# Optimization experiments

Hardware: AMD Instinct MI355X
Metric: run time of the kernel (lower is better)

Reference implementation:

```python
import jax, jax.numpy as jnp
import numpy as np

N = 20000          # nodes
DEG = 8            # deterministic in-degree per node
E = N * DEG        # edges
IN_DIM = 16
HID = 128
EDGE_DIM = 8
OUT_DIM = 4
LN_EPS = 1e-5
# degree histogram has all mass at DEG -> avg log-degree = log(DEG + 1)
AVG_DEG_LOG = float(np.log(DEG + 1.0))


def _init(key, fan_in, fan_out):
    s = float(np.sqrt(2.0 / (fan_in + fan_out)))  # glorot-ish
    return jax.random.normal(key, (fan_in, fan_out), jnp.float32) * s


def setup_inputs() -> dict:
    key = jax.random.key(0)
    ks = jax.random.split(key, 24)
    x = jax.random.normal(ks[0], (N, IN_DIM), jnp.float32)
    src = jax.random.randint(ks[1], (E,), 0, N, jnp.int32)
    dst = (jnp.arange(E, dtype=jnp.int32) % N)  # every node has exactly DEG in-edges
    edge_index = jnp.stack([src, dst], axis=0)
    edge_attr = jax.random.normal(ks[2], (E, EDGE_DIM), jnp.float32)
    d = {"x": x, "edge_attr": edge_attr, "edge_index": edge_index}
    i = 3
    for l, fi in enumerate([IN_DIM, HID]):  # 2 PNAConv layers (num_layers=3)
        d[f"ew{l}"] = _init(ks[i], EDGE_DIM, fi); i += 1   # edge_encoder
        d[f"eb{l}"] = jnp.zeros((fi,), jnp.float32)
        d[f"pw{l}"] = _init(ks[i], 3 * fi, fi); i += 1     # pre_nn: cat(x_i,x_j,e)
        d[f"pb{l}"] = jnp.zeros((fi,), jnp.float32)
        d[f"qw{l}"] = _init(ks[i], 13 * fi, HID); i += 1   # post_nn: (4 aggr * 3 scalers + 1)*F_in
        d[f"qb{l}"] = jnp.zeros((HID,), jnp.float32)
        d[f"lw{l}"] = _init(ks[i], HID, HID); i += 1       # PNAConv.lin
        d[f"lb{l}"] = jnp.zeros((HID,), jnp.float32)
        d[f"g{l}"] = jnp.ones((HID,), jnp.float32)         # LayerNorm gamma
        d[f"b{l}"] = jnp.zeros((HID,), jnp.float32)        # LayerNorm beta
    d["hw"] = _init(ks[i], HID, OUT_DIM)
    d["hb"] = jnp.zeros((OUT_DIM,), jnp.float32)
    return d


def _pna_conv(x, src, dst, edge_attr, ew, eb, pw, pb, qw, qb, lw, lb):
    # messages: cat(x_i, x_j, edge_encoder(edge_attr)) -> pre MLP
    e = edge_attr @ ew + eb                                   # [E, F_in]
    h = jnp.concatenate([x[dst], x[src], e], axis=-1)         # [E, 3*F_in]
    h = h @ pw + pb                                           # [E, F_in]
    # multi-aggregator reduce by destination node
    deg = jax.ops.segment_sum(jnp.ones((E,), h.dtype), dst, num_segments=N)
    degc = jnp.maximum(deg, 1.0)[:, None]
    mean = jax.ops.segment_sum(h, dst, num_segments=N) / degc
    mean2 = jax.ops.segment_sum(h * h, dst, num_segments=N) / degc
    mx = jax.ops.segment_max(h, dst, num_segments=N)
    mn = jax.ops.segment_min(h, dst, num_segments=N)
    std = jnp.sqrt(jax.nn.relu(mean2 - mean * mean) + 1e-5)
    agg = jnp.concatenate([mean, mx, mn, std], axis=-1)       # [N, 4*F_in]
    # degree scalers: identity, amplification, attenuation (scaler-major layout)
    logd = jnp.log(deg + 1.0)[:, None]
    scaled = jnp.concatenate(
        [agg, agg * (logd / AVG_DEG_LOG), agg * (AVG_DEG_LOG / logd)], axis=-1
    )                                                         # [N, 12*F_in]
    out = jnp.concatenate([x, scaled], axis=-1) @ qw + qb     # post_nn, [N, F_out]
    return out @ lw + lb                                      # PNAConv.lin


def _ln(x, g, b):
    m = jnp.mean(x, axis=-1, keepdims=True)
    v = jnp.mean((x - m) ** 2, axis=-1, keepdims=True)
    return (x - m) / jnp.sqrt(v + LN_EPS) * g + b


def reference(x, edge_attr, ew0, eb0, pw0, pb0, qw0, qb0, lw0, lb0, g0, b0,
              ew1, eb1, pw1, pb1, qw1, qb1, lw1, lb1, g1, b1, hw, hb, edge_index):
    src, dst = edge_index[0], edge_index[1]
    h = _pna_conv(x, src, dst, edge_attr, ew0, eb0, pw0, pb0, qw0, qb0, lw0, lb0)
    h = jax.nn.relu(_ln(h, g0, b0))  # dropout is identity at inference
    h = _pna_conv(h, src, dst, edge_attr, ew1, eb1, pw1, pb1, qw1, qb1, lw1, lb1)
    h = jax.nn.relu(_ln(h, g1, b1))
    return h @ hw + hb               # head, [N, OUT_DIM]
```

## Files before the change

### kernel.cpp

```cpp
#include <hip/hip_runtime.h>
#include <math.h>

#define N_NODES 20000
#define N_EDGES 160000

typedef unsigned short ushort_t;
typedef __attribute__((ext_vector_type(8))) short short8v;
typedef __attribute__((ext_vector_type(4))) float f32x4;

#define WS_We0  0
#define WS_b0m  128
#define WS_W0   256
#define WS_b0   10496
#define WS_We1  10624
#define WS_b1m  11648
#define WS_b1   11776
#define WS_WP1  11904
#define WS_WPTU 52864
#define WS_t0   69248
#define WS_u0   389248
#define WS_h0b  709248
#define WS_t1   1989248
#define WS_u1   4549248
#define WS_A0   7109248
#define WS_A1   7109248

__device__ inline ushort_t f2bf(float f) {
    union { float f; unsigned u; } v; v.f = f;
    unsigned r = v.u + 0x7FFFu + ((v.u >> 16) & 1u);
    return (ushort_t)(r >> 16);
}
__device__ inline float bf2f(short s) {
    union { unsigned u; float f; } v; v.u = ((unsigned)(ushort_t)s) << 16; return v.f;
}

__device__ __attribute__((noinline)) void prep_item(
    int tid, const float* __restrict__ x,
    const float* __restrict__ ew0, const float* __restrict__ eb0,
    const float* __restrict__ pw0, const float* __restrict__ pb0,
    const float* __restrict__ qw0, const float* __restrict__ qb0,
    const float* __restrict__ lw0, const float* __restrict__ lb0,
    const float* __restrict__ ew1, const float* __restrict__ eb1,
    const float* __restrict__ pw1, const float* __restrict__ pb1,
    const float* __restrict__ qw1, const float* __restrict__ qb1,
    const float* __restrict__ lw1, const float* __restrict__ lb1,
    float* __restrict__ ws)
{
    if (tid < 81920) {
        int r = tid >> 7, o = tid & 127;
        float acc = 0.f;
        for (int h = 0; h < 128; ++h) {
            float qr;
            if (r < 128) qr = qw1[r*128 + h];
            else {
                int s = r - 128;
                qr = qw1[(128+s)*128+h] + qw1[(640+s)*128+h] + qw1[(1152+s)*128+h];
            }
            acc += qr * lw1[h*128 + o];
        }
        int ct = o >> 4, ks = r >> 5;
        int l = (o & 15) | (((r >> 3) & 3) << 4);
        ((ushort_t*)(ws + WS_WP1))[(size_t)(((ct*20 + ks)*64) + l)*8 + (r & 7)] = f2bf(acc);
    } else if (tid < 82048) {
        int o = tid - 81920;
        float acc = lb1[o];
        for (int h = 0; h < 128; ++h) acc += qb1[h] * lw1[h*128 + o];
        ws[WS_b1 + o] = acc;
    } else if (tid < 92288) {
        int idx = tid - 82048; int r = idx >> 7, o = idx & 127;
        float acc = 0.f;
        for (int h = 0; h < 128; ++h) {
            float qr;
            if (r < 16) qr = qw0[r*128 + h];
            else {
                int s = r - 16;
                qr = qw0[(16+s)*128+h] + qw0[(80+s)*128+h] + qw0[(144+s)*128+h];
            }
            acc += qr * lw0[h*128 + o];
        }
        ws[WS_W0 + idx] = acc;
    } else if (tid < 92416) {
        int o = tid - 92288;
        float acc = lb0[o];
        for (int h = 0; h < 128; ++h) acc += qb0[h] * lw0[h*128 + o];
        ws[WS_b0 + o] = acc;
    } else if (tid < 93440) {
        int idx = tid - 92416; int c = idx >> 7, f = idx & 127;
        float acc = 0.f;
        for (int k = 0; k < 128; ++k) acc += ew1[c*128 + k] * pw1[(256+k)*128 + f];
        ws[WS_We1 + idx] = acc;
    } else if (tid < 93568) {
        int f = tid - 93440;
        float acc = pb1[f];
        for (int k = 0; k < 128; ++k) acc += eb1[k] * pw1[(256+k)*128 + f];
        ws[WS_b1m + f] = acc;
    } else if (tid < 93696) {
        int idx = tid - 93568; int c = idx >> 4, f = idx & 15;
        float acc = 0.f;
        for (int k = 0; k < 16; ++k) acc += ew0[c*16 + k] * pw0[(32+k)*16 + f];
        ws[WS_We0 + idx] = acc;
    } else if (tid < 93712) {
        int f = tid - 93696;
        float acc = pb0[f];
        for (int k = 0; k < 16; ++k) acc += eb0[k] * pw0[(32+k)*16 + f];
        ws[WS_b0m + f] = acc;
    } else if (tid < 126480) {
        int idx = tid - 93712;
        int r = idx >> 7, o = idx & 127;
        int part = r >> 7, rk = r & 127;
        int ct = part*8 + (o >> 4);
        int l = (o & 15) | (((rk >> 3) & 3) << 4);
        ((ushort_t*)(ws + WS_WPTU))[(size_t)(((ct*4 + (rk >> 5))*64) + l)*8 + (rk & 7)]
            = f2bf(pw1[r*128 + o]);
    } else if (tid < 446480) {
        int idx = tid - 126480; int i = idx >> 4, f = idx & 15;
        float acc = 0.f;
        for (int k = 0; k < 16; ++k) acc += x[i*16 + k] * pw0[k*16 + f];
        ws[WS_t0 + idx] = acc;
    } else if (tid < 766480) {
        int idx = tid - 446480; int i = idx >> 4, f = idx & 15;
        float acc = 0.f;
        for (int k = 0; k < 16; ++k) acc += x[i*16 + k] * pw0[(16+k)*16 + f];
        ws[WS_u0 + idx] = acc;
    }
}

__device__ __attribute__((noinline)) void agg0_tile(
    int tile, int t, const float* __restrict__ x, const float* __restrict__ ea,
    const int* __restrict__ src, float* __restrict__ ws)
{
    static __shared__ float ea_s0[16*8*8];
    static __shared__ int   src_s0[16*8];
    static __shared__ float We0_s0[128];
    static __shared__ float b0m_s0[16];
    const int i0 = tile * 16;
    __syncthreads();

    for (int idx = t; idx < 1024; idx += 256) {
        int k = idx >> 7; int rem = idx & 127; int n = rem >> 3, c = rem & 7;
        ea_s0[(n*8 + k)*8 + c] = ea[(i0 + n + k*N_NODES)*8 + c];
    }
    if (t < 128) {
        int k = t >> 4, n = t & 15;
        src_s0[n*8 + k] = src[i0 + n + k*N_NODES];
        We0_s0[t] = ws[WS_We0 + t];
    }
    if (t < 16) b0m_s0[t] = ws[WS_b0m + t];
    __syncthreads();

    const int n = t >> 4, f = t & 15;
    const int i = i0 + n;
    float base = ws[WS_t0 + i*16 + f] + b0m_s0[f];
    float s = 0.f, q = 0.f, mx = -1e30f, mn = 1e30f;
    for (int k = 0; k < 8; ++k) {
        int sj = src_s0[n*8 + k];
        float m = base + ws[WS_u0 + sj*16 + f];
        #pragma unroll
        for (int c = 0; c < 8; ++c) m += ea_s0[(n*8+k)*8 + c] * We0_s0[c*16 + f];
        s += m; q += m*m; mx = fmaxf(mx, m); mn = fminf(mn, m);
    }
    float mean = s * 0.125f, mean2 = q * 0.125f;
    float sd = sqrtf(fmaxf(mean2 - mean*mean, 0.f) + 1e-5f);
    float* A0 = ws + WS_A0 + (size_t)i * 80;
    A0[f]      = x[i*16 + f];
    A0[16 + f] = mean;
    A0[32 + f] = mx;
    A0[48 + f] = mn;
    A0[64 + f] = sd;
}

__device__ __attribute__((noinline)) void gemm0_tile(
    int tile, int t, const float* __restrict__ g0, const float* __restrict__ bln0,
    float* __restrict__ ws)
{
    static __shared__ float As[32][81];
    const int r0 = tile * 32;
    __syncthreads();
    const float* A = ws + WS_A0 + (size_t)r0 * 80;
    for (int idx = t; idx < 32*80; idx += 256) {
        int r = idx / 80, k = idx - r*80;
        As[r][k] = A[idx];
    }
    __syncthreads();
    const int tc = t & 31, tr = t >> 5;
    const int c0 = tc * 4;
    float acc[4][4] = {};
    const float* W = ws + WS_W0;
    #pragma unroll 4
    for (int k = 0; k < 80; ++k) {
        float4 b = *(const float4*)(W + k*128 + c0);
        #pragma unroll
        for (int rr = 0; rr < 4; ++rr) {
            float a = As[tr*4 + rr][k];
            acc[rr][0] += a*b.x; acc[rr][1] += a*b.y;
            acc[rr][2] += a*b.z; acc[rr][3] += a*b.w;
        }
    }
    float4 bias = *(const float4*)(ws + WS_b0 + c0);
    float4 g  = *(const float4*)(g0 + c0);
    float4 bb = *(const float4*)(bln0 + c0);
    ushort_t* h0b = (ushort_t*)(ws + WS_h0b);
    #pragma unroll
    for (int rr = 0; rr < 4; ++rr) {
        float v0 = acc[rr][0] + bias.x, v1 = acc[rr][1] + bias.y;
        float v2 = acc[rr][2] + bias.z, v3 = acc[rr][3] + bias.w;
        float sum = v0+v1+v2+v3;
        float sq  = v0*v0+v1*v1+v2*v2+v3*v3;
        #pragma unroll
        for (int off = 1; off < 32; off <<= 1) {
            sum += __shfl_xor(sum, off, 64);
            sq  += __shfl_xor(sq,  off, 64);
        }
        float mean = sum * (1.f/128.f);
        float var  = sq  * (1.f/128.f) - mean*mean;
        float rstd = rsqrtf(var + 1e-5f);
        ushort4 ob;
        ob.x = f2bf(fmaxf((v0-mean)*rstd*g.x + bb.x, 0.f));
        ob.y = f2bf(fmaxf((v1-mean)*rstd*g.y + bb.y, 0.f));
        ob.z = f2bf(fmaxf((v2-mean)*rstd*g.z + bb.z, 0.f));
        ob.w = f2bf(fmaxf((v3-mean)*rstd*g.w + bb.w, 0.f));
        *(ushort4*)(h0b + (size_t)(r0 + tr*4 + rr)*128 + c0) = ob;
    }
}

__device__ __attribute__((noinline)) void tu1_half(
    int tile, int part, int lane, float* __restrict__ ws)
{
    const int rowbase = tile * 16;
    const ushort_t* h0b = (const ushort_t*)(ws + WS_h0b);
    const ushort_t* WP  = (const ushort_t*)(ws + WS_WPTU);
    const int lr = lane & 15, lk = lane >> 4;
    const size_t arow = rowbase + lr;
    f32x4 acc[8];
    #pragma unroll
    for (int c = 0; c < 8; ++c) acc[c] = (f32x4){0.f,0.f,0.f,0.f};

    #pragma unroll
    for (int ks = 0; ks < 4; ++ks) {
        short8v a = *(const short8v*)(h0b + arow*128 + ks*32 + lk*8);
        #pragma unroll
        for (int c = 0; c < 8; ++c) {
            short8v b = *(const short8v*)(WP + ((size_t)((part*8 + c)*4 + ks)*64 + lane)*8);
            acc[c] = __builtin_amdgcn_mfma_f32_16x16x32_bf16(a, b, acc[c], 0, 0, 0);
        }
    }
    if (part == 0) {
        float* t1 = ws + WS_t1;
        #pragma unroll
        for (int c = 0; c < 8; ++c) {
            int cb = c*16 + lr;
            #pragma unroll
            for (int r = 0; r < 4; ++r) {
                int row = rowbase + lk*4 + r;
                t1[(size_t)row*128 + cb] = acc[c][r];
            }
        }
    } else {
        ushort_t* u1b = (ushort_t*)(ws + WS_u1);
        #pragma unroll
        for (int c = 0; c < 8; ++c) {
            int cb = c*16 + lr;
            #pragma unroll
            for (int r = 0; r < 4; ++r) {
                int row = rowbase + lk*4 + r;
                u1b[(size_t)row*128 + cb] = f2bf(acc[c][r]);
            }
        }
    }
}

__device__ __attribute__((noinline)) void agg1_tile(
    int tile, int t, const float* __restrict__ ea, const int* __restrict__ src,
    float* __restrict__ ws)
{
    static __shared__ float ea_s1[16*8*8];
    static __shared__ int   src_s1[128];
    static __shared__ float We1_s1[1024];
    static __shared__ float b1m_s1[128];
    const int i0 = tile * 16;
    __syncthreads();

    for (int idx = t; idx < 1024; idx += 256) {
        int k = idx >> 7; int rem = idx & 127; int n = rem >> 3, c = rem & 7;
        ea_s1[(n*8 + k)*8 + c] = ea[(i0 + n + k*N_NODES)*8 + c];
    }
    if (t < 128) {
        int k = t >> 4, n = t & 15;
        src_s1[n*8 + k] = src[i0 + n + k*N_NODES];
    }
    for (int idx = t; idx < 1024; idx += 256) We1_s1[idx] = ws[WS_We1 + idx];
    if (t < 128) b1m_s1[t] = ws[WS_b1m + t];
    __syncthreads();

    const int n = t >> 4, f0 = (t & 15) * 8;
    const int i = i0 + n;
    const ushort_t* u1b = (const ushort_t*)(ws + WS_u1);
    float base[8], sm[8], sq[8], mx[8], mn[8];
    #pragma unroll
    for (int e = 0; e < 8; ++e) {
        base[e] = ws[WS_t1 + (size_t)i*128 + f0 + e] + b1m_s1[f0 + e];
        sm[e] = 0.f; sq[e] = 0.f; mx[e] = -1e30f; mn[e] = 1e30f;
    }
    for (int k = 0; k < 8; ++k) {
        int sj = src_s1[n*8 + k];
        short8v uv = *(const short8v*)(u1b + (size_t)sj*128 + f0);
        float m[8];
        #pragma unroll
        for (int e = 0; e < 8; ++e) m[e] = base[e] + bf2f(uv[e]);
        #pragma unroll
        for (int c = 0; c < 8; ++c) {
            float a = ea_s1[(n*8 + k)*8 + c];
            #pragma unroll
            for (int e = 0; e < 8; ++e) m[e] += a * We1_s1[c*128 + f0 + e];
        }
        #pragma unroll
        for (int e = 0; e < 8; ++e) {
            sm[e] += m[e]; sq[e] += m[e]*m[e];
            mx[e] = fmaxf(mx[e], m[e]); mn[e] = fminf(mn[e], m[e]);
        }
    }
    ushort_t* A1 = (ushort_t*)(ws + WS_A1);
    short8v vm, vx, vn, vs;
    #pragma unroll
    for (int e = 0; e < 8; ++e) {
        float mean = sm[e]*0.125f, m2 = sq[e]*0.125f;
        float sd = sqrtf(fmaxf(m2 - mean*mean, 0.f) + 1e-5f);
        vm[e] = (short)f2bf(mean);
        vx[e] = (short)f2bf(mx[e]);
        vn[e] = (short)f2bf(mn[e]);
        vs[e] = (short)f2bf(sd);
    }
    size_t b = (size_t)i*512 + f0;
    *(short8v*)(A1 + b)       = vm;
    *(short8v*)(A1 + b + 128) = vx;
    *(short8v*)(A1 + b + 256) = vn;
    *(short8v*)(A1 + b + 384) = vs;
}

struct KArgs {
    const float *x, *ea; const int* src;
    const float *ew0,*eb0,*pw0,*pb0,*qw0,*qb0,*lw0,*lb0,*g0,*bl0;
    const float *ew1,*eb1,*pw1,*pb1,*qw1,*qb1,*lw1,*lb1,*g1,*bl1;
    const float *hw,*hb;
    float* ws; float* out;
};

__global__ __launch_bounds__(256) void k_prep(KArgs a) {
    int tid = blockIdx.x*256 + threadIdx.x;
    prep_item(tid, a.x, a.ew0, a.eb0, a.pw0, a.pb0, a.qw0, a.qb0, a.lw0, a.lb0,
              a.ew1, a.eb1, a.pw1, a.pb1, a.qw1, a.qb1, a.lw1, a.lb1, a.ws);
}

__global__ __launch_bounds__(256) void k_mid(KArgs a) {
    const int b = blockIdx.x, t = threadIdx.x;
    agg0_tile(b*2,     t, a.x, a.ea, a.src, a.ws);
    agg0_tile(b*2 + 1, t, a.x, a.ea, a.src, a.ws);
    gemm0_tile(b, t, a.g0, a.bl0, a.ws);
    __syncthreads();
    const int w = t >> 6;
    tu1_half(b*2 + (w >> 1), w & 1, t & 63, a.ws);
}

__global__ __launch_bounds__(256) void k_agg1(KArgs a) {
    agg1_tile(blockIdx.x, threadIdx.x, a.ea, a.src, a.ws);
}

__global__ __launch_bounds__(256) void k_gemm1(KArgs a) {
    static __shared__ float redS[2][2][16], redQ[2][2][16];
    static __shared__ f32x4 redP[2][16];
    const int b = blockIdx.x, t = threadIdx.x;
    float* ws = a.ws;
    const int w = t >> 6, lane = t & 63;
    const int rt = w >> 1, chalf = w & 1;
    const int lr = lane & 15, lk = lane >> 4;
    const int rowbase = b * 32;
    const int row = rowbase + rt*16 + lr;
    const ushort_t* h0b = (const ushort_t*)(ws + WS_h0b);
    const ushort_t* A1  = (const ushort_t*)(ws + WS_A1);
    const ushort_t* WP  = (const ushort_t*)(ws + WS_WP1);
    const size_t aoff_h = (size_t)row*128 + lk*8;
    const size_t aoff_a = (size_t)row*512 + lk*8;

    f32x4 acc[4];
    #pragma unroll
    for (int c = 0; c < 4; ++c) acc[c] = (f32x4){0.f,0.f,0.f,0.f};

    short8v aN = *(const short8v*)(h0b + aoff_h);
    short8v bN0 = *(const short8v*)(WP + (size_t)(((chalf*4+0)*20)*64 + lane)*8);
    short8v bN1 = *(const short8v*)(WP + (size_t)(((chalf*4+1)*20)*64 + lane)*8);
    short8v bN2 = *(const short8v*)(WP + (size_t)(((chalf*4+2)*20)*64 + lane)*8);
    short8v bN3 = *(const short8v*)(WP + (size_t)(((chalf*4+3)*20)*64 + lane)*8);
    #pragma unroll
    for (int ksu = 0; ksu < 20; ++ksu) {
        short8v av = aN, bv0 = bN0, bv1 = bN1, bv2 = bN2, bv3 = bN3;
        if (ksu < 19) {
            const int kn = ksu + 1;
            aN = (kn < 4) ? *(const short8v*)(h0b + aoff_h + kn*32)
                          : *(const short8v*)(A1 + aoff_a + (kn-4)*32);
            bN0 = *(const short8v*)(WP + (size_t)(((chalf*4+0)*20 + kn)*64 + lane)*8);
            bN1 = *(const short8v*)(WP + (size_t)(((chalf*4+1)*20 + kn)*64 + lane)*8);
            bN2 = *(const short8v*)(WP + (size_t)(((chalf*4+2)*20 + kn)*64 + lane)*8);
            bN3 = *(const short8v*)(WP + (size_t)(((chalf*4+3)*20 + kn)*64 + lane)*8);
        }
        acc[0] = __builtin_amdgcn_mfma_f32_16x16x32_bf16(av, bv0, acc[0], 0, 0, 0);
        acc[1] = __builtin_amdgcn_mfma_f32_16x16x32_bf16(av, bv1, acc[1], 0, 0, 0);
        acc[2] = __builtin_amdgcn_mfma_f32_16x16x32_bf16(av, bv2, acc[2], 0, 0, 0);
        acc[3] = __builtin_amdgcn_mfma_f32_16x16x32_bf16(av, bv3, acc[3], 0, 0, 0);
    }

    float bc[4], gc[4], bbc[4]; f32x4 hwc[4];
    #pragma unroll
    for (int c = 0; c < 4; ++c) {
        int col = (chalf*4 + c)*16 + lr;
        bc[c]  = ws[WS_b1 + col];
        gc[c]  = a.g1[col];
        bbc[c] = a.bl1[col];
        hwc[c] = *(const f32x4*)(a.hw + col*4);
    }

    #pragma unroll
    for (int r = 0; r < 4; ++r) {
        float s = 0.f, q = 0.f;
        #pragma unroll
        for (int c = 0; c < 4; ++c) {
            float v = acc[c][r] + bc[c];
            s += v; q += v*v;
        }
        #pragma unroll
        for (int off = 1; off < 16; off <<= 1) {
            s += __shfl_xor(s, off, 64);
            q += __shfl_xor(q, off, 64);
        }
        if (lr == 0) { redS[rt][chalf][lk*4 + r] = s; redQ[rt][chalf][lk*4 + r] = q; }
    }
    __syncthreads();

    f32x4 poarr[4];
    #pragma unroll
    for (int r = 0; r < 4; ++r) {
        int orow = lk*4 + r;
        float s_tot = redS[rt][0][orow] + redS[rt][1][orow];
        float q_tot = redQ[rt][0][orow] + redQ[rt][1][orow];
        float mean = s_tot * (1.f/128.f);
        float var  = q_tot * (1.f/128.f) - mean*mean;
        float rstd = rsqrtf(var + 1e-5f);
        f32x4 po = (f32x4){0.f,0.f,0.f,0.f};
        #pragma unroll
        for (int c = 0; c < 4; ++c) {
            float v = acc[c][r] + bc[c];
            float o = fmaxf((v-mean)*rstd*gc[c] + bbc[c], 0.f);
            po += o * hwc[c];
        }
        #pragma unroll
        for (int off = 1; off < 16; off <<= 1) {
            po.x += __shfl_xor(po.x, off, 64);
            po.y += __shfl_xor(po.y, off, 64);
            po.z += __shfl_xor(po.z, off, 64);
            po.w += __shfl_xor(po.w, off, 64);
        }
        poarr[r] = po;
        if (chalf == 1 && lr == 0) redP[rt][orow] = po;
    }
    __syncthreads();

    if (chalf == 0 && lr == 0) {
        f32x4 hb4 = *(const f32x4*)a.hb;
        #pragma unroll
        for (int r = 0; r < 4; ++r) {
            int orow = lk*4 + r;
            f32x4 res = poarr[r] + redP[rt][orow] + hb4;
            *(f32x4*)(a.out + (size_t)(rowbase + rt*16 + orow)*4) = res;
        }
    }
}

extern "C" void kernel_launch(void* const* d_in, const int* in_sizes, int n_in,
                              void* d_out, int out_size, void* d_ws, size_t ws_size,
                              hipStream_t stream)
{
    KArgs a;
    a.x    = (const float*)d_in[0];
    a.ea   = (const float*)d_in[1];
    a.src  = (const int*)d_in[2];
    a.ew0  = (const float*)d_in[3];
    a.eb0  = (const float*)d_in[4];
    a.pw0  = (const float*)d_in[5];
    a.pb0  = (const float*)d_in[6];
    a.qw0  = (const float*)d_in[7];
    a.qb0  = (const float*)d_in[8];
    a.lw0  = (const float*)d_in[9];
    a.lb0  = (const float*)d_in[10];
    a.g0   = (const float*)d_in[11];
    a.bl0  = (const float*)d_in[12];
    a.ew1  = (const float*)d_in[13];
    a.eb1  = (const float*)d_in[14];
    a.pw1  = (const float*)d_in[15];
    a.pb1  = (const float*)d_in[16];
    a.qw1  = (const float*)d_in[17];
    a.qb1  = (const float*)d_in[18];
    a.lw1  = (const float*)d_in[19];
    a.lb1  = (const float*)d_in[20];
    a.g1   = (const float*)d_in[21];
    a.bl1  = (const float*)d_in[22];
    a.hw   = (const float*)d_in[23];
    a.hb   = (const float*)d_in[24];
    a.ws   = (float*)d_ws;
    a.out  = (float*)d_out;

    k_prep <<<2995, 256, 0, stream>>>(a);
    k_mid  <<< 625, 256, 0, stream>>>(a);
    k_agg1 <<<1250, 256, 0, stream>>>(a);
    k_gemm1<<< 625, 256, 0, stream>>>(a);
}
```

Baseline: 99.46 us.

## Compute layer-0 node projections on the fly and move weight prep into agg1

Drops the precomputed per-node t0/u0 projections from the prep kernel. agg0 now gathers neighbor x rows into shared memory and multiplies them by pw0 inline, which removes the workspace round-trip and most of the prep launch. The large weight-folding prep items (the first 82048, used only by the final GEMM) are spread across k_agg1 blocks so the prep kernel shrinks to 174 blocks. The cost is extra redundant FLOPs in agg0 and some load imbalance added to agg1 threads.

```diff
diff --git a/kernel.cpp b/kernel.cpp
--- a/kernel.cpp
+++ b/kernel.cpp
@@ -17,8 +17,6 @@
 #define WS_b1   11776
 #define WS_WP1  11904
 #define WS_WPTU 52864
-#define WS_t0   69248
-#define WS_u0   389248
 #define WS_h0b  709248
 #define WS_t1   1989248
 #define WS_u1   4549248
@@ -35,7 +33,7 @@
 }
 
 __device__ __attribute__((noinline)) void prep_item(
-    int tid, const float* __restrict__ x,
+    int tid,
     const float* __restrict__ ew0, const float* __restrict__ eb0,
     const float* __restrict__ pw0, const float* __restrict__ pb0,
     const float* __restrict__ qw0, const float* __restrict__ qb0,
@@ -112,27 +110,22 @@
         int l = (o & 15) | (((rk >> 3) & 3) << 4);
         ((ushort_t*)(ws + WS_WPTU))[(size_t)(((ct*4 + (rk >> 5))*64) + l)*8 + (rk & 7)]
             = f2bf(pw1[r*128 + o]);
-    } else if (tid < 446480) {
-        int idx = tid - 126480; int i = idx >> 4, f = idx & 15;
-        float acc = 0.f;
-        for (int k = 0; k < 16; ++k) acc += x[i*16 + k] * pw0[k*16 + f];
-        ws[WS_t0 + idx] = acc;
-    } else if (tid < 766480) {
-        int idx = tid - 446480; int i = idx >> 4, f = idx & 15;
-        float acc = 0.f;
-        for (int k = 0; k < 16; ++k) acc += x[i*16 + k] * pw0[(16+k)*16 + f];
-        ws[WS_u0 + idx] = acc;
-    }
-}
-
-__device__ __attribute__((noinline)) void agg0_tile(
+    }
+}
+
+__device__ __attribute__((noinline)) void agg0_fly(
     int tile, int t, const float* __restrict__ x, const float* __restrict__ ea,
-    const int* __restrict__ src, float* __restrict__ ws)
+    const int* __restrict__ src, const float* __restrict__ pw0,
+    float* __restrict__ ws)
 {
     static __shared__ float ea_s0[16*8*8];
     static __shared__ int   src_s0[16*8];
     static __shared__ float We0_s0[128];
     static __shared__ float b0m_s0[16];
+    static __shared__ float pw0a_s[256];
+    static __shared__ float pw0b_s[256];
+    static __shared__ float xn_s[256];
+    static __shared__ float xg_s[2048];
     const int i0 = tile * 16;
     __syncthreads();
 
@@ -146,15 +139,32 @@
         We0_s0[t] = ws[WS_We0 + t];
     }
     if (t < 16) b0m_s0[t] = ws[WS_b0m + t];
+    {
+        pw0a_s[t] = pw0[t];
+        pw0b_s[t] = pw0[256 + t];
+        int n = t >> 4, k = t & 15;
+        xn_s[t] = x[(size_t)(i0 + n)*16 + k];
+    }
+    __syncthreads();
+
+    for (int idx = t; idx < 2048; idx += 256) {
+        int n = idx >> 7; int rem = idx & 127; int k = rem >> 4, c = rem & 15;
+        xg_s[idx] = x[(size_t)src_s0[n*8 + k]*16 + c];
+    }
     __syncthreads();
 
     const int n = t >> 4, f = t & 15;
     const int i = i0 + n;
-    float base = ws[WS_t0 + i*16 + f] + b0m_s0[f];
+    float t0v = 0.f;
+    #pragma unroll
+    for (int k = 0; k < 16; ++k) t0v += xn_s[n*16 + k] * pw0a_s[k*16 + f];
+    float base = t0v + b0m_s0[f];
     float s = 0.f, q = 0.f, mx = -1e30f, mn = 1e30f;
     for (int k = 0; k < 8; ++k) {
-        int sj = src_s0[n*8 + k];
-        float m = base + ws[WS_u0 + sj*16 + f];
+        float uv = 0.f;
+        #pragma unroll
+        for (int c = 0; c < 16; ++c) uv += xg_s[(n*8 + k)*16 + c] * pw0b_s[c*16 + f];
+        float m = base + uv;
         #pragma unroll
         for (int c = 0; c < 8; ++c) m += ea_s0[(n*8+k)*8 + c] * We0_s0[c*16 + f];
         s += m; q += m*m; mx = fmaxf(mx, m); mn = fminf(mn, m);
@@ -162,7 +172,7 @@
     float mean = s * 0.125f, mean2 = q * 0.125f;
     float sd = sqrtf(fmaxf(mean2 - mean*mean, 0.f) + 1e-5f);
     float* A0 = ws + WS_A0 + (size_t)i * 80;
-    A0[f]      = x[i*16 + f];
+    A0[f]      = xn_s[n*16 + f];
     A0[16 + f] = mean;
     A0[32 + f] = mx;
     A0[48 + f] = mn;
@@ -346,15 +356,16 @@
 };
 
 __global__ __launch_bounds__(256) void k_prep(KArgs a) {
-    int tid = blockIdx.x*256 + threadIdx.x;
-    prep_item(tid, a.x, a.ew0, a.eb0, a.pw0, a.pb0, a.qw0, a.qb0, a.lw0, a.lb0,
-              a.ew1, a.eb1, a.pw1, a.pb1, a.qw1, a.qb1, a.lw1, a.lb1, a.ws);
+    int tid = 82048 + blockIdx.x*256 + threadIdx.x;
+    if (tid < 126480)
+        prep_item(tid, a.ew0, a.eb0, a.pw0, a.pb0, a.qw0, a.qb0, a.lw0, a.lb0,
+                  a.ew1, a.eb1, a.pw1, a.pb1, a.qw1, a.qb1, a.lw1, a.lb1, a.ws);
 }
 
 __global__ __launch_bounds__(256) void k_mid(KArgs a) {
     const int b = blockIdx.x, t = threadIdx.x;
-    agg0_tile(b*2,     t, a.x, a.ea, a.src, a.ws);
-    agg0_tile(b*2 + 1, t, a.x, a.ea, a.src, a.ws);
+    agg0_fly(b*2,     t, a.x, a.ea, a.src, a.pw0, a.ws);
+    agg0_fly(b*2 + 1, t, a.x, a.ea, a.src, a.pw0, a.ws);
     gemm0_tile(b, t, a.g0, a.bl0, a.ws);
     __syncthreads();
     const int w = t >> 6;
@@ -363,6 +374,10 @@
 
 __global__ __launch_bounds__(256) void k_agg1(KArgs a) {
     agg1_tile(blockIdx.x, threadIdx.x, a.ea, a.src, a.ws);
+    int item = blockIdx.x * 66 + threadIdx.x;
+    if (threadIdx.x < 66 && item < 82048)
+        prep_item(item, a.ew0, a.eb0, a.pw0, a.pb0, a.qw0, a.qb0, a.lw0, a.lb0,
+                  a.ew1, a.eb1, a.pw1, a.pb1, a.qw1, a.qb1, a.lw1, a.lb1, a.ws);
 }
 
 __global__ __launch_bounds__(256) void k_gemm1(KArgs a) {
@@ -507,7 +522,7 @@
     a.ws   = (float*)d_ws;
     a.out  = (float*)d_out;
 
-    k_prep <<<2995, 256, 0, stream>>>(a);
+    k_prep <<< 174, 256, 0, stream>>>(a);
     k_mid  <<< 625, 256, 0, stream>>>(a);
     k_agg1 <<<1250, 256, 0, stream>>>(a);
     k_gemm1<<< 625, 256, 0, stream>>>(a);
```

Measured after the change: 147.7 us. 48.5% more time.
